# Kernel tuning notes

Hardware: AMD Instinct MI355X
Metric: run time of the kernel (lower is better)

Reference implementation:

```python
import jax, jax.numpy as jnp
import numpy as np

B, L, HID = 2, 4096, 2048
H, KVH, D = 32, 8, 64          # heads, kv heads, head_dim
G = H // KVH                   # GQA groups = 4
W = 512                        # window == max_bias_length
NB = L // W                    # number of query blocks
THETA = 10000.0
SCALE = 1.0 / np.sqrt(D)


def setup_inputs() -> dict:
    key = jax.random.key(0)
    ks = jax.random.split(key, 8)
    s = 0.02
    return {
        "hidden_states": jax.random.normal(ks[0], (B, L, HID), jnp.float32),
        "Wq": jax.random.normal(ks[1], (HID, HID), jnp.float32) * s,
        "Wk": jax.random.normal(ks[2], (KVH * D, HID), jnp.float32) * s,
        "Wv": jax.random.normal(ks[3], (KVH * D, HID), jnp.float32) * s,
        "Wo": jax.random.normal(ks[4], (HID, HID), jnp.float32) * s,
        "bias": jax.random.normal(ks[5], (H, W), jnp.float32) * s,   # per-head relative-position bias
        "tau": jnp.full((H,), -1.0, jnp.float32) + 0.1 * jax.random.normal(ks[6], (H,), jnp.float32),
    }


def _rope(x, pos):
    # non-interleaved (rotate-half) RoPE over full head_dim
    d = x.shape[-1]
    inv = 1.0 / (THETA ** (jnp.arange(0, d, 2, dtype=jnp.float32) / d))
    ang = pos[:, None] * inv                     # [L, d/2]
    cos = jnp.cos(ang)[None, :, None, :]
    sin = jnp.sin(ang)[None, :, None, :]
    x1, x2 = jnp.split(x, 2, axis=-1)
    return jnp.concatenate([x1 * cos - x2 * sin, x2 * cos + x1 * sin], axis=-1)


def reference(hidden_states, Wq, Wk, Wv, Wo, bias, tau):
    # QKV projections (nn.Linear: y = x @ W.T)
    q = (hidden_states @ Wq.T).reshape(B, L, H, D)
    k = (hidden_states @ Wk.T).reshape(B, L, KVH, D)
    v = (hidden_states @ Wv.T).reshape(B, L, KVH, D)

    pos = jnp.arange(L, dtype=jnp.float32)
    q = _rope(q, pos)
    k = _rope(k, pos)

    # GQA expansion (repeat_interleave over head dim)
    k = jnp.repeat(k, G, axis=2)
    v = jnp.repeat(v, G, axis=2)

    # [B,H,NB,W,D] blocks; each query block attends to its own + previous key block
    q = q.transpose(0, 2, 1, 3).reshape(B, H, NB, W, D)
    k = k.transpose(0, 2, 1, 3).reshape(B, H, NB, W, D)
    v = v.transpose(0, 2, 1, 3).reshape(B, H, NB, W, D)
    zpad = jnp.zeros((B, H, 1, W, D), k.dtype)
    kk = jnp.concatenate([jnp.concatenate([zpad, k[:, :, :-1]], 2), k], 3)  # [B,H,NB,2W,D]
    vv = jnp.concatenate([jnp.concatenate([zpad, v[:, :, :-1]], 2), v], 3)

    qi = jnp.arange(W)
    ki = jnp.arange(2 * W)
    rel = qi[:, None] - ki[None, :] + W                       # i - j in [0, W) when valid
    jglob = jnp.arange(NB)[:, None, None] * W + (ki - W)[None, None, :]
    mask = (rel >= 0) & (rel < W) & (jglob >= 0)              # [NB, W, 2W]
    bias_g = bias[:, jnp.clip(rel, 0, W - 1)]                 # [H, W, 2W]

    s = jnp.einsum('bhnqd,bhnkd->bhnqk', q, kk) * SCALE + bias_g[None, :, None]
    s = jnp.where(mask[None, None], s, -1e30)

    # lazy softmax: per-head learnable sink logit tau in the denominator
    m = jnp.maximum(s.max(-1), tau[None, :, None, None])      # [B,H,NB,W]
    p = jnp.exp(s - m[..., None])
    denom = jnp.exp(tau[None, :, None, None] - m) + p.sum(-1)
    o = jnp.einsum('bhnqk,bhnkd->bhnqd', p, vv) / denom[..., None]

    o = o.reshape(B, H, L, D).transpose(0, 2, 1, 3).reshape(B, L, HID)
    return o @ Wo.T
```

## Files before the change

### kernel.cpp

```cpp
#include <hip/hip_runtime.h>
#include <hip/hip_bf16.h>

typedef __attribute__((ext_vector_type(8))) short short8;
typedef __attribute__((ext_vector_type(4))) float f32x4;

#define DI __device__ __forceinline__

DI unsigned short f2b(float x) {
    unsigned int u = __builtin_bit_cast(unsigned int, x);
    u += 0x7FFFu + ((u >> 16) & 1u);
    return (unsigned short)(u >> 16);
}

DI void gload_lds16(const void* g, void* l) {
    __builtin_amdgcn_global_load_lds(
        (const __attribute__((address_space(1))) void*)g,
        (__attribute__((address_space(3))) void*)l, 16, 0, 0);
}

__global__ __launch_bounds__(256) void cvt_bf16(const float* __restrict__ src,
                                                unsigned short* __restrict__ dst, int n8) {
    int i = blockIdx.x * blockDim.x + threadIdx.x;
    if (i >= n8) return;
    const float4* s = (const float4*)src + 2 * (size_t)i;
    float4 a = s[0], b = s[1];
    short8 o;
    o[0] = (short)f2b(a.x); o[1] = (short)f2b(a.y); o[2] = (short)f2b(a.z); o[3] = (short)f2b(a.w);
    o[4] = (short)f2b(b.x); o[5] = (short)f2b(b.y); o[6] = (short)f2b(b.z); o[7] = (short)f2b(b.w);
    *(short8*)(dst + 8 * (size_t)i) = o;
}

__global__ __launch_bounds__(256) void trig_tab(float2* __restrict__ cs) {
    int idx = blockIdx.x * blockDim.x + threadIdx.x;
    if (idx >= 4096 * 32) return;
    int pos = idx >> 5, i = idx & 31;
    double inv = exp(-(double)i * (9.210340371976184 / 32.0));
    double a = (double)pos * inv;
    cs[idx] = make_float2((float)cos(a), (float)sin(a));
}

template <int EPI>
__global__ __launch_bounds__(256) void gemm128(const unsigned short* __restrict__ A,
                                               const unsigned short* __restrict__ Bw,
                                               float* __restrict__ Cout,
                                               unsigned short* __restrict__ q_bf,
                                               unsigned short* __restrict__ k_bf,
                                               unsigned short* __restrict__ v_bf,
                                               const float2* __restrict__ cs) {
    constexpr int K = 2048;
    __shared__ unsigned short At[128 * 32];
    __shared__ unsigned short Bt[128 * 32];
    const int tid = threadIdx.x;
    const int lane = tid & 63, w = tid >> 6;
    const int wm = w >> 1, wn = w & 1;
    const int bm = blockIdx.x, bn = blockIdx.y;
    const int r16 = lane & 15, hi = lane >> 4;
    const int rowc = tid >> 2, slotc = tid & 3;

    f32x4 acc[4][4] = {};

    for (int kt = 0; kt < K / 32; ++kt) {
        __syncthreads();
#pragma unroll
        for (int p = 0; p < 2; ++p) {
            int row = p * 64 + rowc;
            gload_lds16(A + (long)(bm * 128 + row) * K + kt * 32 + slotc * 8,
                        (char*)At + p * 4096 + w * 1024);
            gload_lds16(Bw + (long)(bn * 128 + row) * K + kt * 32 + slotc * 8,
                        (char*)Bt + p * 4096 + w * 1024);
        }
        asm volatile("s_waitcnt vmcnt(0)" ::: "memory");
        __syncthreads();
        short8 af[4], bfr[4];
#pragma unroll
        for (int mf = 0; mf < 4; ++mf)
            af[mf] = *(const short8*)(At + (wm * 64 + mf * 16 + r16) * 32 + hi * 8);
#pragma unroll
        for (int nf = 0; nf < 4; ++nf)
            bfr[nf] = *(const short8*)(Bt + (wn * 64 + nf * 16 + r16) * 32 + hi * 8);
#pragma unroll
        for (int mf = 0; mf < 4; ++mf)
#pragma unroll
            for (int nf = 0; nf < 4; ++nf)
                acc[mf][nf] = __builtin_amdgcn_mfma_f32_16x16x32_bf16(af[mf], bfr[nf], acc[mf][nf], 0, 0, 0);
    }

    if (EPI == 0) {
#pragma unroll
        for (int mf = 0; mf < 4; ++mf)
#pragma unroll
            for (int r = 0; r < 4; ++r) {
                long row = (long)bm * 128 + wm * 64 + mf * 16 + hi * 4 + r;
                float* o = Cout + row * 2048 + bn * 128 + wn * 64 + r16;
                o[0] = acc[mf][0][r]; o[16] = acc[mf][1][r]; o[32] = acc[mf][2][r]; o[48] = acc[mf][3][r];
            }
    } else {
        const int colBase = bn * 128 + wn * 64;
        const int b = bm >> 5;
        unsigned short* dst;
        bool dorope;
        if (colBase < 2048)      { dst = q_bf + (long)(b * 32 + (colBase >> 6)) * 4096 * 64; dorope = true; }
        else if (colBase < 2560) { dst = k_bf + (long)(b * 8 + ((colBase - 2048) >> 6)) * 4096 * 64; dorope = true; }
        else                     { dst = v_bf + (long)(b * 8 + ((colBase - 2560) >> 6)) * 4096 * 64; dorope = false; }
#pragma unroll
        for (int mf = 0; mf < 4; ++mf)
#pragma unroll
            for (int r = 0; r < 4; ++r) {
                int pos = (bm * 128 + wm * 64 + mf * 16 + hi * 4 + r) & 4095;
                if (dorope) {
#pragma unroll
                    for (int nf = 0; nf < 2; ++nf) {
                        int i = nf * 16 + r16;
                        float2 c2 = cs[pos * 32 + i];
                        float x1 = acc[mf][nf][r], x2 = acc[mf][nf + 2][r];
                        dst[(long)pos * 64 + i]      = f2b(x1 * c2.x - x2 * c2.y);
                        dst[(long)pos * 64 + 32 + i] = f2b(x2 * c2.x + x1 * c2.y);
                    }
                } else {
#pragma unroll
                    for (int nf = 0; nf < 4; ++nf)
                        dst[(long)pos * 64 + nf * 16 + r16] = f2b(acc[mf][nf][r]);
                }
            }
    }
}

__global__ __launch_bounds__(256) void transpose_v(const unsigned short* __restrict__ v,
                                                   unsigned short* __restrict__ vT) {
    __shared__ unsigned short t[64][65];
    const int plane = blockIdx.y;
    const int p0 = blockIdx.x * 64;
    const int tid = threadIdx.x;
    const int rr = tid >> 2, c0 = (tid & 3) * 16;
    const unsigned short* src = v + (long)plane * 4096 * 64 + (long)(p0 + rr) * 64 + c0;
    short8 x0 = *(const short8*)src, x1 = *(const short8*)(src + 8);
#pragma unroll
    for (int j = 0; j < 8; ++j) t[rr][c0 + j] = (unsigned short)x0[j];
#pragma unroll
    for (int j = 0; j < 8; ++j) t[rr][c0 + 8 + j] = (unsigned short)x1[j];
    __syncthreads();
    short8 o0, o1;
#pragma unroll
    for (int j = 0; j < 8; ++j) o0[j] = (short)t[c0 + j][rr];
#pragma unroll
    for (int j = 0; j < 8; ++j) o1[j] = (short)t[c0 + 8 + j][rr];
    unsigned short* d = vT + (long)plane * 64 * 4096 + (long)rr * 4096 + p0 + c0;
    *(short8*)d = o0;
    *(short8*)(d + 8) = o1;
}

__global__ __launch_bounds__(512, 2) void attn_kernel(const unsigned short* __restrict__ q_bf,
                                                      const unsigned short* __restrict__ k_bf,
                                                      const unsigned short* __restrict__ v_bfT,
                                                      const float* __restrict__ bias,
                                                      const float* __restrict__ tau,
                                                      unsigned short* __restrict__ o_bf) {
    __shared__ unsigned short Kt[64 * 64];
    __shared__ unsigned short Vt[64 * 64];
    __shared__ unsigned short Pl[8][640];
    __shared__ float bias_l[512];

    const int nb = blockIdx.x, h = blockIdx.y, b = blockIdx.z;
    const int kvh = h >> 2;
    const int tid = threadIdx.x;
    const int lane = tid & 63, w = tid >> 6;
    const int r16 = lane & 15, hi = lane >> 4;

    bias_l[tid] = bias[h * 512 + tid];
    const float tauh = tau[h];

    const unsigned short* qp = q_bf + ((long)(b * 32 + h) * 4096 + nb * 512) * 64;
    const unsigned short* kp = k_bf + (long)(b * 8 + kvh) * 4096 * 64;
    const unsigned short* vp = v_bfT + (long)(b * 8 + kvh) * 64 * 4096;
    const int k0 = nb * 512 - 512;

    short8 aq[4][2];
#pragma unroll
    for (int mf = 0; mf < 4; ++mf) {
        int mq = w * 16 + mf * 128;
#pragma unroll
        for (int dk = 0; dk < 2; ++dk)
            aq[mf][dk] = *(const short8*)(qp + (long)(mq + r16) * 64 + dk * 32 + hi * 8);
    }

    f32x4 oacc[4][4] = {};
    float psum[4][4] = {};

    const int srow = tid >> 3, sslot = tid & 7;
    const int swz = sslot ^ (srow & 7);
    unsigned short* plw = Pl[w];

    for (int t = 0; t < 16; ++t) {
        if (nb == 0 && t < 8) continue;
        __syncthreads();
        {
            int jr = k0 + t * 64 + srow; if (jr < 0) jr = 0;
            gload_lds16(kp + (long)jr * 64 + swz * 8, (char*)Kt + w * 1024);
            int jc = k0 + t * 64 + swz * 8; if (jc < 0) jc = 0;
            gload_lds16(vp + (long)srow * 4096 + jc, (char*)Vt + w * 1024);
        }
        asm volatile("s_waitcnt vmcnt(0)" ::: "memory");
        __syncthreads();

        short8 bk[4][2], vb[4][2];
#pragma unroll
        for (int nf = 0; nf < 4; ++nf) {
            int rowK = nf * 16 + r16;
            int xo = (rowK & 7) << 4;
#pragma unroll
            for (int ks = 0; ks < 2; ++ks) {
                bk[nf][ks] = *(const short8*)((const char*)Kt + rowK * 128 + ((hi * 16 + ks * 64) ^ xo));
                vb[nf][ks] = *(const short8*)((const char*)Vt + rowK * 128 + ((hi * 16 + ks * 64) ^ xo));
            }
        }

#pragma unroll
        for (int mf = 0; mf < 4; ++mf) {
            const int mq = w * 16 + mf * 128;
            bool valid = (t * 64 + 63 > mq) && (t * 64 <= mq + 527);
            if (!valid) continue;
#pragma unroll
            for (int half = 0; half < 2; ++half) {
#pragma unroll
                for (int nn = 0; nn < 2; ++nn) {
                    const int nfs = half * 2 + nn;
                    f32x4 s = {};
                    __builtin_amdgcn_s_setprio(1);
                    s = __builtin_amdgcn_mfma_f32_16x16x32_bf16(aq[mf][0], bk[nfs][0], s, 0, 0, 0);
                    s = __builtin_amdgcn_mfma_f32_16x16x32_bf16(aq[mf][1], bk[nfs][1], s, 0, 0, 0);
                    __builtin_amdgcn_s_setprio(0);
                    const int kkl = t * 64 + nfs * 16 + r16;
#pragma unroll
                    for (int r = 0; r < 4; ++r) {
                        const int q = mq + hi * 4 + r;
                        const int rel = q - kkl + 512;
                        bool ok = (rel >= 0) && (rel < 512) && (nb > 0 || kkl >= 512);
                        int relc = rel < 0 ? 0 : (rel > 511 ? 511 : rel);
                        float sv = ok ? (s[r] * 0.125f + bias_l[relc]) : -1e30f;
                        float pv = __expf(sv);
                        psum[mf][r] += pv;
                        plw[(hi * 4 + r) * 40 + nn * 16 + r16] = f2b(pv);
                    }
                }
                short8 pa;
                __builtin_memcpy(&pa, plw + r16 * 40 + hi * 8, 16);
                __builtin_amdgcn_s_setprio(1);
#pragma unroll
                for (int nfd = 0; nfd < 4; ++nfd)
                    oacc[mf][nfd] = __builtin_amdgcn_mfma_f32_16x16x32_bf16(pa, vb[nfd][half], oacc[mf][nfd], 0, 0, 0);
                __builtin_amdgcn_s_setprio(0);
            }
        }
    }

#pragma unroll
    for (int mf = 0; mf < 4; ++mf)
#pragma unroll
        for (int r = 0; r < 4; ++r) {
            float v = psum[mf][r];
            v += __shfl_xor(v, 1); v += __shfl_xor(v, 2);
            v += __shfl_xor(v, 4); v += __shfl_xor(v, 8);
            psum[mf][r] = v + __expf(tauh);
        }

#pragma unroll
    for (int mf = 0; mf < 4; ++mf) {
        const int mq = w * 16 + mf * 128;
#pragma unroll
        for (int r = 0; r < 4; ++r) {
            const long tok = (long)b * 4096 + nb * 512 + mq + hi * 4 + r;
            const float rdn = 1.0f / psum[mf][r];
#pragma unroll
            for (int nfd = 0; nfd < 4; ++nfd)
                o_bf[tok * 2048 + h * 64 + nfd * 16 + r16] = f2b(oacc[mf][nfd][r] * rdn);
        }
    }
}

extern "C" void kernel_launch(void* const* d_in, const int* in_sizes, int n_in,
                              void* d_out, int out_size, void* d_ws, size_t ws_size,
                              hipStream_t stream) {
    const float* hs   = (const float*)d_in[0];
    const float* Wq   = (const float*)d_in[1];
    const float* Wk   = (const float*)d_in[2];
    const float* Wv   = (const float*)d_in[3];
    const float* Wo   = (const float*)d_in[4];
    const float* bias = (const float*)d_in[5];
    const float* tau  = (const float*)d_in[6];
    float* out = (float*)d_out;

    char* p = (char*)d_ws;
    auto alloc = [&](size_t bytes) { char* r = p; p += (bytes + 255) & ~(size_t)255; return r; };
    unsigned short* hs_bf = (unsigned short*)alloc(8192UL * 2048 * 2);
    unsigned short* w1_bf = (unsigned short*)alloc(3072UL * 2048 * 2);
    unsigned short* wo_bf = (unsigned short*)alloc(2048UL * 2048 * 2);
    unsigned short* q_bf  = (unsigned short*)alloc(64UL * 4096 * 64 * 2);
    unsigned short* k_bf  = (unsigned short*)alloc(16UL * 4096 * 64 * 2);
    unsigned short* v_bf  = (unsigned short*)alloc(16UL * 4096 * 64 * 2);
    unsigned short* v_bfT = (unsigned short*)alloc(16UL * 4096 * 64 * 2);
    float2* cs = (float2*)alloc(4096UL * 32 * 8);
    unsigned short* o_bf = hs_bf;
    if ((size_t)(p - (char*)d_ws) > ws_size) return;

    cvt_bf16<<<8192, 256, 0, stream>>>(hs, hs_bf, 16777216 / 8);
    cvt_bf16<<<2048, 256, 0, stream>>>(Wq, w1_bf, 4194304 / 8);
    cvt_bf16<<<512, 256, 0, stream>>>(Wk, w1_bf + 2048UL * 2048, 1048576 / 8);
    cvt_bf16<<<512, 256, 0, stream>>>(Wv, w1_bf + 2560UL * 2048, 1048576 / 8);
    cvt_bf16<<<2048, 256, 0, stream>>>(Wo, wo_bf, 4194304 / 8);
    trig_tab<<<512, 256, 0, stream>>>(cs);
    gemm128<1><<<dim3(64, 24), 256, 0, stream>>>(hs_bf, w1_bf, nullptr, q_bf, k_bf, v_bf, cs);
    transpose_v<<<dim3(64, 16), 256, 0, stream>>>(v_bf, v_bfT);
    attn_kernel<<<dim3(8, 32, 2), 512, 0, stream>>>(q_bf, k_bf, v_bfT, bias, tau, o_bf);
    gemm128<0><<<dim3(64, 16), 256, 0, stream>>>(o_bf, wo_bf, out, nullptr, nullptr, nullptr, nullptr);
}
```

Baseline: 557.5 us.

## Double-buffer LDS tiles in GEMM and attention to overlap loads with MFMA

```diff
diff --git a/kernel.cpp b/kernel.cpp
--- a/kernel.cpp
+++ b/kernel.cpp
@@ -48,8 +48,9 @@
                                                unsigned short* __restrict__ v_bf,
                                                const float2* __restrict__ cs) {
     constexpr int K = 2048;
-    __shared__ unsigned short At[128 * 32];
-    __shared__ unsigned short Bt[128 * 32];
+    constexpr int NT = K / 32;
+    __shared__ unsigned short At[2][128 * 32];
+    __shared__ unsigned short Bt[2][128 * 32];
     const int tid = threadIdx.x;
     const int lane = tid & 63, w = tid >> 6;
     const int wm = w >> 1, wn = w & 1;
@@ -59,30 +60,43 @@
 
     f32x4 acc[4][4] = {};
 
-    for (int kt = 0; kt < K / 32; ++kt) {
-        __syncthreads();
+    auto stage = [&](int t, int b) {
 #pragma unroll
         for (int p = 0; p < 2; ++p) {
             int row = p * 64 + rowc;
-            gload_lds16(A + (long)(bm * 128 + row) * K + kt * 32 + slotc * 8,
-                        (char*)At + p * 4096 + w * 1024);
-            gload_lds16(Bw + (long)(bn * 128 + row) * K + kt * 32 + slotc * 8,
-                        (char*)Bt + p * 4096 + w * 1024);
-        }
-        asm volatile("s_waitcnt vmcnt(0)" ::: "memory");
-        __syncthreads();
+            gload_lds16(A + (long)(bm * 128 + row) * K + t * 32 + slotc * 8,
+                        (char*)At[b] + p * 4096 + w * 1024);
+            gload_lds16(Bw + (long)(bn * 128 + row) * K + t * 32 + slotc * 8,
+                        (char*)Bt[b] + p * 4096 + w * 1024);
+        }
+    };
+
+    stage(0, 0);
+    stage(1, 1);
+    asm volatile("s_waitcnt vmcnt(4)" ::: "memory");
+    __builtin_amdgcn_s_barrier();
+
+    for (int t = 0; t < NT; ++t) {
+        const int b = t & 1;
         short8 af[4], bfr[4];
 #pragma unroll
         for (int mf = 0; mf < 4; ++mf)
-            af[mf] = *(const short8*)(At + (wm * 64 + mf * 16 + r16) * 32 + hi * 8);
+            af[mf] = *(const short8*)(At[b] + (wm * 64 + mf * 16 + r16) * 32 + hi * 8);
 #pragma unroll
         for (int nf = 0; nf < 4; ++nf)
-            bfr[nf] = *(const short8*)(Bt + (wn * 64 + nf * 16 + r16) * 32 + hi * 8);
+            bfr[nf] = *(const short8*)(Bt[b] + (wn * 64 + nf * 16 + r16) * 32 + hi * 8);
+        asm volatile("s_waitcnt lgkmcnt(0)" ::: "memory");
+        __builtin_amdgcn_s_barrier();
+        const bool more = (t + 2 < NT);
+        if (more) stage(t + 2, b);
 #pragma unroll
         for (int mf = 0; mf < 4; ++mf)
 #pragma unroll
             for (int nf = 0; nf < 4; ++nf)
                 acc[mf][nf] = __builtin_amdgcn_mfma_f32_16x16x32_bf16(af[mf], bfr[nf], acc[mf][nf], 0, 0, 0);
+        if (more) { asm volatile("s_waitcnt vmcnt(4)" ::: "memory"); }
+        else      { asm volatile("s_waitcnt vmcnt(0)" ::: "memory"); }
+        __builtin_amdgcn_s_barrier();
     }
 
     if (EPI == 0) {
@@ -155,8 +169,8 @@
                                                       const float* __restrict__ bias,
                                                       const float* __restrict__ tau,
                                                       unsigned short* __restrict__ o_bf) {
-    __shared__ unsigned short Kt[64 * 64];
-    __shared__ unsigned short Vt[64 * 64];
+    __shared__ unsigned short Kt[2][64 * 64];
+    __shared__ unsigned short Vt[2][64 * 64];
     __shared__ unsigned short Pl[8][640];
     __shared__ float bias_l[512];
 
@@ -190,18 +204,21 @@
     const int swz = sslot ^ (srow & 7);
     unsigned short* plw = Pl[w];
 
-    for (int t = 0; t < 16; ++t) {
-        if (nb == 0 && t < 8) continue;
-        __syncthreads();
-        {
-            int jr = k0 + t * 64 + srow; if (jr < 0) jr = 0;
-            gload_lds16(kp + (long)jr * 64 + swz * 8, (char*)Kt + w * 1024);
-            int jc = k0 + t * 64 + swz * 8; if (jc < 0) jc = 0;
-            gload_lds16(vp + (long)srow * 4096 + jc, (char*)Vt + w * 1024);
-        }
-        asm volatile("s_waitcnt vmcnt(0)" ::: "memory");
-        __syncthreads();
-
+    auto stageKV = [&](int t, int bb) {
+        int jr = k0 + t * 64 + srow; if (jr < 0) jr = 0;
+        gload_lds16(kp + (long)jr * 64 + swz * 8, (char*)Kt[bb] + w * 1024);
+        int jc = k0 + t * 64 + swz * 8; if (jc < 0) jc = 0;
+        gload_lds16(vp + (long)srow * 4096 + jc, (char*)Vt[bb] + w * 1024);
+    };
+
+    const int t0 = (nb == 0) ? 8 : 0;
+    stageKV(t0, 0);
+    stageKV(t0 + 1, 1);
+    asm volatile("s_waitcnt vmcnt(2) lgkmcnt(0)" ::: "memory");
+    __builtin_amdgcn_s_barrier();
+
+    for (int t = t0; t < 16; ++t) {
+        const int bb = t & 1;
         short8 bk[4][2], vb[4][2];
 #pragma unroll
         for (int nf = 0; nf < 4; ++nf) {
@@ -209,10 +226,14 @@
             int xo = (rowK & 7) << 4;
 #pragma unroll
             for (int ks = 0; ks < 2; ++ks) {
-                bk[nf][ks] = *(const short8*)((const char*)Kt + rowK * 128 + ((hi * 16 + ks * 64) ^ xo));
-                vb[nf][ks] = *(const short8*)((const char*)Vt + rowK * 128 + ((hi * 16 + ks * 64) ^ xo));
+                bk[nf][ks] = *(const short8*)((const char*)Kt[bb] + rowK * 128 + ((hi * 16 + ks * 64) ^ xo));
+                vb[nf][ks] = *(const short8*)((const char*)Vt[bb] + rowK * 128 + ((hi * 16 + ks * 64) ^ xo));
             }
         }
+        asm volatile("s_waitcnt lgkmcnt(0)" ::: "memory");
+        __builtin_amdgcn_s_barrier();
+        const bool more = (t + 2 < 16);
+        if (more) stageKV(t + 2, bb);
 
 #pragma unroll
         for (int mf = 0; mf < 4; ++mf) {
@@ -251,6 +272,9 @@
                 __builtin_amdgcn_s_setprio(0);
             }
         }
+        if (more) { asm volatile("s_waitcnt vmcnt(2)" ::: "memory"); }
+        else      { asm volatile("s_waitcnt vmcnt(0)" ::: "memory"); }
+        __builtin_amdgcn_s_barrier();
     }
 
 #pragma unroll
```

Result: faster. 528.7 us (-5.2%).
